# Optimization experiments

Measured on AMD Instinct MI355X. Metric: run time of the kernel, lower is better.

Reference implementation:

```python
import jax, jax.numpy as jnp
import numpy as np
import math

D_MODEL = 1024
H = 16
D_K = D_MODEL // H
SEQ = 4096
NEG = -1000000000.0  # mask constant from the original code


def setup_inputs() -> dict:
    key = jax.random.key(0)
    ks = jax.random.split(key, 7)
    return {
        "Q": jax.random.normal(ks[0], (SEQ, D_MODEL), dtype=jnp.float32),
        "K": jax.random.normal(ks[1], (SEQ, D_MODEL), dtype=jnp.float32),
        "V": jax.random.normal(ks[2], (SEQ, D_MODEL), dtype=jnp.float32),
        "W_Q": jax.random.normal(ks[3], (H, D_MODEL, D_K), dtype=jnp.float32),
        "W_K": jax.random.normal(ks[4], (H, D_MODEL, D_K), dtype=jnp.float32),
        "W_V": jax.random.normal(ks[5], (H, D_MODEL, D_K), dtype=jnp.float32),
        "W_O": jax.random.normal(ks[6], (D_MODEL, D_MODEL), dtype=jnp.float32),
        "mask": 1,
    }


def reference(Q, K, V, W_Q, W_K, W_V, W_O, mask):
    d_k = W_Q.shape[-1]
    s = Q.shape[0]
    # batched per-head projections: [h, s, d_k]
    Qh = jnp.einsum("sd,hdk->hsk", Q, W_Q)
    Kh = jnp.einsum("sd,hdk->hsk", K, W_K)
    Vh = jnp.einsum("sd,hdk->hsk", V, W_V)
    # scores: [h, s_q, s_k]
    scores = jnp.einsum("hqk,hsk->hqs", Qh, Kh) / math.sqrt(d_k)
    if mask:
        # faithful to torch: tril(scores) + triu(ones, 1) * -1e9
        lower = jnp.tril(jnp.ones((s, s), dtype=scores.dtype))
        upper = jnp.triu(jnp.ones((s, s), dtype=scores.dtype), k=1)
        scores = scores * lower + upper * NEG
    attn = jax.nn.softmax(scores, axis=-1)
    heads = jnp.einsum("hqs,hsk->hqk", attn, Vh)  # [h, s, d_k]
    # concat heads along feature dim in head order -> [s, h*d_k]
    concat = jnp.transpose(heads, (1, 0, 2)).reshape(s, -1)
    return concat @ W_O
```

## Files before the change

### kernel.cpp

```cpp
#include <hip/hip_runtime.h>
#include <hip/hip_bf16.h>

constexpr int S      = 4096;
constexpr int DMODEL = 1024;
constexpr int H      = 16;
constexpr int DK     = 64;

typedef __attribute__((ext_vector_type(8))) short          short8;
typedef __attribute__((ext_vector_type(4))) short          short4v;
typedef __attribute__((ext_vector_type(4))) float          float4v;
typedef __attribute__((ext_vector_type(4))) unsigned short ushort4v;
typedef __attribute__((ext_vector_type(8))) unsigned short ushort8;

__device__ __forceinline__ unsigned short f2bf(float x) {
    unsigned u = __builtin_bit_cast(unsigned, x);
    u += 0x7FFFu + ((u >> 16) & 1u);
    return (unsigned short)(u >> 16);
}
__device__ __forceinline__ float bf2f(unsigned short h) {
    unsigned u = ((unsigned)h) << 16;
    return __builtin_bit_cast(float, u);
}

__global__ __launch_bounds__(256) void split_inputs(const float* __restrict__ Q,
                                                    const float* __restrict__ K,
                                                    const float* __restrict__ V,
                                                    unsigned short* __restrict__ QH,
                                                    unsigned short* __restrict__ QL,
                                                    unsigned short* __restrict__ KH,
                                                    unsigned short* __restrict__ KL,
                                                    unsigned short* __restrict__ Vb)
{
    const int z = blockIdx.z;
    const size_t base = ((size_t)blockIdx.x * 256 + threadIdx.x) * 8;
    const float* src = (z == 0) ? Q : (z == 1) ? K : V;
    const float4 a = *(const float4*)(src + base);
    const float4 b = *(const float4*)(src + base + 4);
    const float xs[8] = {a.x, a.y, a.z, a.w, b.x, b.y, b.z, b.w};
    ushort8 hv, lv;
#pragma unroll
    for (int j = 0; j < 8; ++j) {
        const unsigned short h = f2bf(xs[j]);
        hv[j] = h;
        lv[j] = f2bf(xs[j] - bf2f(h));
    }
    if (z == 0)      { *(ushort8*)(QH + base) = hv; *(ushort8*)(QL + base) = lv; }
    else if (z == 1) { *(ushort8*)(KH + base) = hv; *(ushort8*)(KL + base) = lv; }
    else             { *(ushort8*)(Vb + base) = hv; }
}

__global__ __launch_bounds__(256) void conv_k(const float* __restrict__ Kc,
                                              unsigned short* __restrict__ KH,
                                              unsigned short* __restrict__ KL)
{
    const size_t base = ((size_t)blockIdx.x * 256 + threadIdx.x) * 8;
    const float4 a = *(const float4*)(Kc + base);
    const float4 b = *(const float4*)(Kc + base + 4);
    const float xs[8] = {a.x, a.y, a.z, a.w, b.x, b.y, b.z, b.w};
    ushort8 hv, lv;
#pragma unroll
    for (int j = 0; j < 8; ++j) {
        const unsigned short h = f2bf(xs[j]);
        hv[j] = h;
        lv[j] = f2bf(xs[j] - bf2f(h));
    }
    *(ushort8*)(KH + base) = hv;
    *(ushort8*)(KL + base) = lv;
}

__global__ __launch_bounds__(256) void transpose_v(const float* __restrict__ Vc,
                                                   unsigned short* __restrict__ Vt)
{
    __shared__ unsigned short Ts[64][68];
    const int t  = threadIdx.x;
    const int s0 = blockIdx.x * 64;
    const int n0 = blockIdx.y * 64;
#pragma unroll
    for (int i = 0; i < 4; ++i) {
        const int row = (t >> 4) + i * 16;
        const int col = (t & 15) * 4;
        const float4 v = *(const float4*)&Vc[(size_t)(s0 + row) * 1024 + n0 + col];
        Ts[row][col + 0] = f2bf(v.x); Ts[row][col + 1] = f2bf(v.y);
        Ts[row][col + 2] = f2bf(v.z); Ts[row][col + 3] = f2bf(v.w);
    }
    __syncthreads();
#pragma unroll
    for (int i = 0; i < 4; ++i) {
        const int n  = (t >> 4) + i * 16;
        const int sb = (t & 15) * 4;
        ushort4v v;
#pragma unroll
        for (int j = 0; j < 4; ++j) v[j] = Ts[sb + j][n];
        *(ushort4v*)&Vt[(size_t)(n0 + n) * 4096 + s0 + sb] = v;
    }
}

__global__ __launch_bounds__(256) void transpose_w(const float* __restrict__ in,
                                                   unsigned short* __restrict__ oh,
                                                   unsigned short* __restrict__ ol,
                                                   int z_mult, int rstride)
{
    __shared__ float Ts[64][65];
    const int t  = threadIdx.x;
    const int z  = blockIdx.z;
    const int r0 = blockIdx.x * 64;
    const float* src = in + (size_t)z * z_mult;
#pragma unroll
    for (int i = 0; i < 4; ++i) {
        const int row = (t >> 4) + i * 16;
        const int col = (t & 15) * 4;
        const float4 v = *(const float4*)&src[(size_t)(r0 + row) * rstride + col];
        Ts[row][col + 0] = v.x; Ts[row][col + 1] = v.y;
        Ts[row][col + 2] = v.z; Ts[row][col + 3] = v.w;
    }
    __syncthreads();
#pragma unroll
    for (int i = 0; i < 4; ++i) {
        const int c  = (t >> 4) + i * 16;
        const int rb = (t & 15) * 4;
        ushort4v hv, lv;
#pragma unroll
        for (int j = 0; j < 4; ++j) {
            const float x = Ts[rb + j][c];
            const unsigned short h = f2bf(x);
            hv[j] = h;
            lv[j] = f2bf(x - bf2f(h));
        }
        const size_t o = (size_t)(z * 64 + c) * 1024 + r0 + rb;
        *(ushort4v*)&oh[o] = hv;
        if (ol) *(ushort4v*)&ol[o] = lv;
    }
}

template <bool SPLIT>
__device__ __forceinline__ void gemm_core(unsigned short* __restrict__ sm,
                                          const unsigned short* __restrict__ Ah,
                                          const unsigned short* __restrict__ Al,
                                          const unsigned short* __restrict__ Bh,
                                          const unsigned short* __restrict__ Bl,
                                          float* __restrict__ C,
                                          int m0, int n0)
{
    unsigned short* AsH = sm;
    unsigned short* BsH = sm + 4096;
    unsigned short* AsL = sm + 8192;
    unsigned short* BsL = sm + 12288;

    const int t    = threadIdx.x;
    const int wave = t >> 6;
    const int lane = t & 63;
    const int quad = lane >> 4;
    const int l15  = lane & 15;
    const int wm   = (wave & 1) * 64;
    const int wn   = (wave >> 1) * 64;

    float4v acc[4][4];
#pragma unroll
    for (int mi = 0; mi < 4; ++mi)
#pragma unroll
        for (int ni = 0; ni < 4; ++ni)
#pragma unroll
            for (int r = 0; r < 4; ++r) acc[mi][ni][r] = 0.f;

    for (int k0 = 0; k0 < 1024; k0 += 32) {
        __syncthreads();
#pragma unroll
        for (int i = 0; i < 2; ++i) {
            const int c   = t + 256 * i;
            const int row = c >> 2;
            const int kc  = (c & 3) * 8;
            *(ushort8*)&AsH[row * 32 + kc] =
                *(const ushort8*)&Ah[(size_t)(m0 + row) * 1024 + k0 + kc];
            *(ushort8*)&BsH[row * 32 + kc] =
                *(const ushort8*)&Bh[(size_t)(n0 + row) * 1024 + k0 + kc];
            if (SPLIT) {
                *(ushort8*)&AsL[row * 32 + kc] =
                    *(const ushort8*)&Al[(size_t)(m0 + row) * 1024 + k0 + kc];
                *(ushort8*)&BsL[row * 32 + kc] =
                    *(const ushort8*)&Bl[(size_t)(n0 + row) * 1024 + k0 + kc];
            }
        }
        __syncthreads();

        short8 afh[4], bfh[4], afl[4], bfl[4];
#pragma unroll
        for (int mi = 0; mi < 4; ++mi)
            afh[mi] = *(const short8*)&AsH[(wm + mi * 16 + l15) * 32 + quad * 8];
#pragma unroll
        for (int ni = 0; ni < 4; ++ni)
            bfh[ni] = *(const short8*)&BsH[(wn + ni * 16 + l15) * 32 + quad * 8];
        if (SPLIT) {
#pragma unroll
            for (int mi = 0; mi < 4; ++mi)
                afl[mi] = *(const short8*)&AsL[(wm + mi * 16 + l15) * 32 + quad * 8];
#pragma unroll
            for (int ni = 0; ni < 4; ++ni)
                bfl[ni] = *(const short8*)&BsL[(wn + ni * 16 + l15) * 32 + quad * 8];
        }

#pragma unroll
        for (int mi = 0; mi < 4; ++mi)
#pragma unroll
            for (int ni = 0; ni < 4; ++ni) {
                acc[mi][ni] = __builtin_amdgcn_mfma_f32_16x16x32_bf16(
                    afh[mi], bfh[ni], acc[mi][ni], 0, 0, 0);
                if (SPLIT) {
                    acc[mi][ni] = __builtin_amdgcn_mfma_f32_16x16x32_bf16(
                        afh[mi], bfl[ni], acc[mi][ni], 0, 0, 0);
                    acc[mi][ni] = __builtin_amdgcn_mfma_f32_16x16x32_bf16(
                        afl[mi], bfh[ni], acc[mi][ni], 0, 0, 0);
                }
            }
    }

#pragma unroll
    for (int mi = 0; mi < 4; ++mi)
#pragma unroll
        for (int r = 0; r < 4; ++r) {
            const int m = m0 + wm + mi * 16 + quad * 4 + r;
            float* cp = C + (size_t)m * 1024 + n0 + wn + l15;
#pragma unroll
            for (int ni = 0; ni < 4; ++ni) cp[ni * 16] = acc[mi][ni][r];
        }
}

__global__ __launch_bounds__(256) void proj_mfma(
    const unsigned short* __restrict__ XqH, const unsigned short* __restrict__ XqL,
    const unsigned short* __restrict__ XkH, const unsigned short* __restrict__ XkL,
    const unsigned short* __restrict__ Xv,
    const unsigned short* __restrict__ WqtH, const unsigned short* __restrict__ WqtL,
    const unsigned short* __restrict__ WktH, const unsigned short* __restrict__ WktL,
    const unsigned short* __restrict__ Wvt,
    float* __restrict__ Qc, float* __restrict__ Kc, float* __restrict__ Vc)
{
    __shared__ __align__(16) unsigned short smem[4 * 4096];
    const int m0 = blockIdx.x * 128, n0 = blockIdx.y * 128;
    if (blockIdx.z == 0)
        gemm_core<true>(smem, XqH, XqL, WqtH, WqtL, Qc, m0, n0);
    else if (blockIdx.z == 1)
        gemm_core<true>(smem, XkH, XkL, WktH, WktL, Kc, m0, n0);
    else
        gemm_core<false>(smem, Xv, nullptr, Wvt, nullptr, Vc, m0, n0);
}

__global__ __launch_bounds__(256) void out_gemm_mfma(
    const unsigned short* __restrict__ Ocb,
    const unsigned short* __restrict__ WOt,
    float* __restrict__ out)
{
    __shared__ __align__(16) unsigned short smem[2 * 4096];
    gemm_core<false>(smem, Ocb, nullptr, WOt, nullptr, out,
                     blockIdx.x * 128, blockIdx.y * 128);
}

__global__ __launch_bounds__(256) void attn_mfma(const float* __restrict__ Qc,
                                                 const unsigned short* __restrict__ KHg,
                                                 const unsigned short* __restrict__ KLg,
                                                 const unsigned short* __restrict__ Vtg,
                                                 unsigned short* __restrict__ Ocb)
{
    __shared__ __align__(16) short Khi[64][72];
    __shared__ __align__(16) short Klo[64][72];
    __shared__ __align__(16) short Vts[64][72];
    __shared__ __align__(16) short Pb[4][16][72];

    const int bid = blockIdx.x;
    const int h   = bid & 15;
    const int qt  = 63 - (bid >> 4);
    const int q0  = qt * 64;

    const int t    = threadIdx.x;
    const int wave = t >> 6;
    const int lane = t & 63;
    const int quad = lane >> 4;
    const int l15  = lane & 15;

    short8 qhi[2], qlo[2];
    {
        const int qrow = q0 + wave * 16 + l15;
        const float* qp = Qc + (size_t)qrow * DMODEL + h * 64 + quad * 8;
#pragma unroll
        for (int ks = 0; ks < 2; ++ks) {
            float4 a = *(const float4*)(qp + ks * 32);
            float4 b = *(const float4*)(qp + ks * 32 + 4);
            const float xs[8] = {a.x, a.y, a.z, a.w, b.x, b.y, b.z, b.w};
#pragma unroll
            for (int j = 0; j < 8; ++j) {
                const unsigned short hi = f2bf(xs[j]);
                const unsigned short lo = f2bf(xs[j] - bf2f(hi));
                qhi[ks][j] = (short)hi;
                qlo[ks][j] = (short)lo;
            }
        }
    }

    short8 bones;
    {
        const short ob = (l15 == 0) ? (short)0x3F80 : (short)0;
#pragma unroll
        for (int j = 0; j < 8; ++j) bones[j] = ob;
    }

    float m_r[4] = {-1e30f, -1e30f, -1e30f, -1e30f};
    float4v lacc;
    float4v oacc[4];
#pragma unroll
    for (int r = 0; r < 4; ++r) lacc[r] = 0.f;
#pragma unroll
    for (int nt = 0; nt < 4; ++nt)
#pragma unroll
        for (int r = 0; r < 4; ++r) oacc[nt][r] = 0.f;

    const int srow = t >> 3;
    const int soff = (t & 7) * 8;

    ushort8 kh[2], kl[2], vt[2];
#pragma unroll
    for (int i = 0; i < 2; ++i) {
        const int row = srow + 32 * i;
        kh[i] = *(const ushort8*)&KHg[(size_t)row * 1024 + h * 64 + soff];
        kl[i] = *(const ushort8*)&KLg[(size_t)row * 1024 + h * 64 + soff];
        vt[i] = *(const ushort8*)&Vtg[(size_t)(h * 64 + row) * 4096 + soff];
    }

    for (int jt = 0; jt <= qt; ++jt) {
        const int j0 = jt * 64;
#pragma unroll
        for (int i = 0; i < 2; ++i) {
            const int row = srow + 32 * i;
            *(ushort8*)&Khi[row][soff] = kh[i];
            *(ushort8*)&Klo[row][soff] = kl[i];
            *(ushort8*)&Vts[row][soff] = vt[i];
        }
        __syncthreads();

        if (jt < qt) {
            const int jn = j0 + 64;
#pragma unroll
            for (int i = 0; i < 2; ++i) {
                const int row = srow + 32 * i;
                kh[i] = *(const ushort8*)&KHg[(size_t)(jn + row) * 1024 + h * 64 + soff];
                kl[i] = *(const ushort8*)&KLg[(size_t)(jn + row) * 1024 + h * 64 + soff];
                vt[i] = *(const ushort8*)&Vtg[(size_t)(h * 64 + row) * 4096 + jn + soff];
            }
        }

        float4v sacc[4];
#pragma unroll
        for (int nt = 0; nt < 4; ++nt)
#pragma unroll
            for (int r = 0; r < 4; ++r) sacc[nt][r] = 0.f;
#pragma unroll
        for (int nt = 0; nt < 4; ++nt) {
            const int key = nt * 16 + l15;
#pragma unroll
            for (int ks = 0; ks < 2; ++ks) {
                const short8 bh = *(const short8*)&Khi[key][ks * 32 + quad * 8];
                const short8 bl = *(const short8*)&Klo[key][ks * 32 + quad * 8];
                sacc[nt] = __builtin_amdgcn_mfma_f32_16x16x32_bf16(qhi[ks], bh, sacc[nt], 0, 0, 0);
                sacc[nt] = __builtin_amdgcn_mfma_f32_16x16x32_bf16(qhi[ks], bl, sacc[nt], 0, 0, 0);
                sacc[nt] = __builtin_amdgcn_mfma_f32_16x16x32_bf16(qlo[ks], bh, sacc[nt], 0, 0, 0);
            }
        }

#pragma unroll
        for (int nt = 0; nt < 4; ++nt) {
            const int jg = j0 + nt * 16 + l15;
#pragma unroll
            for (int r = 0; r < 4; ++r) {
                const int qg = q0 + wave * 16 + quad * 4 + r;
                const float v = sacc[nt][r] * 0.125f;
                sacc[nt][r] = (jg > qg) ? -1e9f : v;
            }
        }

        float rmax[4];
#pragma unroll
        for (int r = 0; r < 4; ++r)
            rmax[r] = fmaxf(fmaxf(sacc[0][r], sacc[1][r]), fmaxf(sacc[2][r], sacc[3][r]));
#pragma unroll
        for (int off = 1; off < 16; off <<= 1)
#pragma unroll
            for (int r = 0; r < 4; ++r)
                rmax[r] = fmaxf(rmax[r], __shfl_xor(rmax[r], off));

        float alpha[4];
#pragma unroll
        for (int r = 0; r < 4; ++r) {
            const float mn = fmaxf(m_r[r], rmax[r]);
            alpha[r] = __expf(m_r[r] - mn);
            m_r[r] = mn;
        }

#pragma unroll
        for (int nt = 0; nt < 4; ++nt)
#pragma unroll
            for (int r = 0; r < 4; ++r)
                sacc[nt][r] = __expf(sacc[nt][r] - m_r[r]);

#pragma unroll
        for (int r = 0; r < 4; ++r) lacc[r] *= alpha[r];
#pragma unroll
        for (int nt = 0; nt < 4; ++nt)
#pragma unroll
            for (int r = 0; r < 4; ++r)
                oacc[nt][r] *= alpha[r];

#pragma unroll
        for (int nt = 0; nt < 4; ++nt)
#pragma unroll
            for (int r = 0; r < 4; ++r)
                Pb[wave][quad * 4 + r][nt * 16 + l15] = (short)f2bf(sacc[nt][r]);
        __asm__ volatile("s_waitcnt lgkmcnt(0)" ::: "memory");

        short8 af[2];
        af[0] = *(const short8*)&Pb[wave][l15][quad * 8];
        af[1] = *(const short8*)&Pb[wave][l15][32 + quad * 8];
#pragma unroll
        for (int nt = 0; nt < 4; ++nt) {
            const int dk = nt * 16 + l15;
#pragma unroll
            for (int ks = 0; ks < 2; ++ks) {
                const short8 bv = *(const short8*)&Vts[dk][ks * 32 + quad * 8];
                oacc[nt] = __builtin_amdgcn_mfma_f32_16x16x32_bf16(af[ks], bv, oacc[nt], 0, 0, 0);
            }
        }
        lacc = __builtin_amdgcn_mfma_f32_16x16x32_bf16(af[0], bones, lacc, 0, 0, 0);
        lacc = __builtin_amdgcn_mfma_f32_16x16x32_bf16(af[1], bones, lacc, 0, 0, 0);
        __syncthreads();
    }

#pragma unroll
    for (int r = 0; r < 4; ++r) {
        const float lsum = __shfl(lacc[r], (lane & 48));
        const float inv  = 1.0f / lsum;
        const int qg = q0 + wave * 16 + quad * 4 + r;
        unsigned short* op = Ocb + (size_t)qg * DMODEL + h * 64 + l15;
#pragma unroll
        for (int nt = 0; nt < 4; ++nt)
            op[nt * 16] = f2bf(oacc[nt][r] * inv);
    }
}

extern "C" void kernel_launch(void* const* d_in, const int* in_sizes, int n_in,
                              void* d_out, int out_size, void* d_ws, size_t ws_size,
                              hipStream_t stream)
{
    const float* Q  = (const float*)d_in[0];
    const float* K  = (const float*)d_in[1];
    const float* V  = (const float*)d_in[2];
    const float* WQ = (const float*)d_in[3];
    const float* WK = (const float*)d_in[4];
    const float* WV = (const float*)d_in[5];
    const float* WO = (const float*)d_in[6];

    float* out = (float*)d_out;

    const size_t SD4 = (size_t)S * DMODEL * 4;
    const size_t SD2 = (size_t)S * DMODEL * 2;
    const size_t W2  = (size_t)DMODEL * DMODEL * 2;
    char* p = (char*)d_ws;
    auto take = [&](size_t b) { char* r = p; p += b; return r; };

    float* Qc = (float*)take(SD4);
    float* Kc = (float*)take(SD4);
    float* Vc = (float*)take(SD4);
    unsigned short* XqH = (unsigned short*)take(SD2);
    unsigned short* XqL = (unsigned short*)take(SD2);
    unsigned short* XkH = (unsigned short*)take(SD2);
    unsigned short* XkL = (unsigned short*)take(SD2);
    unsigned short* Xv  = (unsigned short*)take(SD2);
    unsigned short* WqtH = (unsigned short*)take(W2);
    unsigned short* WqtL = (unsigned short*)take(W2);
    unsigned short* WktH = (unsigned short*)take(W2);
    unsigned short* WktL = (unsigned short*)take(W2);
    unsigned short* Wvt  = (unsigned short*)take(W2);
    unsigned short* WOt  = (unsigned short*)take(W2);
    unsigned short* Ocb  = (unsigned short*)take(SD2);
    unsigned short* KHg = XqH;
    unsigned short* KLg = XqL;
    unsigned short* Vtg = Xv;

    split_inputs<<<dim3(2048, 1, 3), 256, 0, stream>>>(Q, K, V,
                                                       XqH, XqL, XkH, XkL, Xv);
    transpose_w<<<dim3(16, 1, 16), 256, 0, stream>>>(WQ, WqtH, WqtL, 65536, 64);
    transpose_w<<<dim3(16, 1, 16), 256, 0, stream>>>(WK, WktH, WktL, 65536, 64);
    transpose_w<<<dim3(16, 1, 16), 256, 0, stream>>>(WV, Wvt, nullptr, 65536, 64);
    transpose_w<<<dim3(16, 1, 16), 256, 0, stream>>>(WO, WOt, nullptr, 64, 1024);
    proj_mfma<<<dim3(S / 128, DMODEL / 128, 3), 256, 0, stream>>>(
        XqH, XqL, XkH, XkL, Xv, WqtH, WqtL, WktH, WktL, Wvt, Qc, Kc, Vc);
    conv_k<<<dim3(2048), 256, 0, stream>>>(Kc, KHg, KLg);
    transpose_v<<<dim3(S / 64, DMODEL / 64), 256, 0, stream>>>(Vc, Vtg);
    attn_mfma<<<dim3((S / 64) * H), 256, 0, stream>>>(Qc, KHg, KLg, Vtg, Ocb);
    out_gemm_mfma<<<dim3(S / 128, DMODEL / 128), 256, 0, stream>>>(Ocb, WOt, out);
}
```

Measured before the change: 355.3 us.

## Use direct global-to-LDS loads in projection GEMM and exp2 softmax

The projection GEMM now stages tiles with global_load_lds, which writes straight into shared memory and skips the register round-trip. The attention kernel folds log2(e) into the score scale so it can use the hardware exp2 instruction. It also applies the causal mask compare only on diagonal tiles, leaving a plain scale multiply elsewhere. The LDS addressing changes from row*32+kc to a per-wave linear layout, which may not match the fragment read pattern unless the two coincide.

```diff
diff --git a/kernel.cpp b/kernel.cpp
--- a/kernel.cpp
+++ b/kernel.cpp
@@ -20,6 +20,13 @@
 __device__ __forceinline__ float bf2f(unsigned short h) {
     unsigned u = ((unsigned)h) << 16;
     return __builtin_bit_cast(float, u);
+}
+__device__ __forceinline__ float fexp2(float x) { return __builtin_amdgcn_exp2f(x); }
+
+__device__ __forceinline__ void gl_lds16(const unsigned short* g, unsigned short* l) {
+    __builtin_amdgcn_global_load_lds(
+        (const __attribute__((address_space(1))) unsigned int*)g,
+        (__attribute__((address_space(3))) unsigned int*)l, 16, 0, 0);
 }
 
 __global__ __launch_bounds__(256) void split_inputs(const float* __restrict__ Q,
@@ -169,15 +176,12 @@
             const int c   = t + 256 * i;
             const int row = c >> 2;
             const int kc  = (c & 3) * 8;
-            *(ushort8*)&AsH[row * 32 + kc] =
-                *(const ushort8*)&Ah[(size_t)(m0 + row) * 1024 + k0 + kc];
-            *(ushort8*)&BsH[row * 32 + kc] =
-                *(const ushort8*)&Bh[(size_t)(n0 + row) * 1024 + k0 + kc];
+            const int lb  = (i * 256 + wave * 64) * 8;
+            gl_lds16(&Ah[(size_t)(m0 + row) * 1024 + k0 + kc], AsH + lb);
+            gl_lds16(&Bh[(size_t)(n0 + row) * 1024 + k0 + kc], BsH + lb);
             if (SPLIT) {
-                *(ushort8*)&AsL[row * 32 + kc] =
-                    *(const ushort8*)&Al[(size_t)(m0 + row) * 1024 + k0 + kc];
-                *(ushort8*)&BsL[row * 32 + kc] =
-                    *(const ushort8*)&Bl[(size_t)(n0 + row) * 1024 + k0 + kc];
+                gl_lds16(&Al[(size_t)(m0 + row) * 1024 + k0 + kc], AsL + lb);
+                gl_lds16(&Bl[(size_t)(n0 + row) * 1024 + k0 + kc], BsL + lb);
             }
         }
         __syncthreads();
@@ -301,6 +305,8 @@
         for (int j = 0; j < 8; ++j) bones[j] = ob;
     }
 
+    constexpr float SCL = 0.18033688011112042f;
+
     float m_r[4] = {-1e30f, -1e30f, -1e30f, -1e30f};
     float4v lacc;
     float4v oacc[4];
@@ -363,15 +369,23 @@
             }
         }
 
-#pragma unroll
-        for (int nt = 0; nt < 4; ++nt) {
-            const int jg = j0 + nt * 16 + l15;
-#pragma unroll
-            for (int r = 0; r < 4; ++r) {
-                const int qg = q0 + wave * 16 + quad * 4 + r;
-                const float v = sacc[nt][r] * 0.125f;
-                sacc[nt][r] = (jg > qg) ? -1e9f : v;
-            }
+        if (jt == qt) {
+#pragma unroll
+            for (int nt = 0; nt < 4; ++nt) {
+                const int jg = j0 + nt * 16 + l15;
+#pragma unroll
+                for (int r = 0; r < 4; ++r) {
+                    const int qg = q0 + wave * 16 + quad * 4 + r;
+                    const float v = sacc[nt][r] * SCL;
+                    sacc[nt][r] = (jg > qg) ? -1e9f : v;
+                }
+            }
+        } else {
+#pragma unroll
+            for (int nt = 0; nt < 4; ++nt)
+#pragma unroll
+                for (int r = 0; r < 4; ++r)
+                    sacc[nt][r] *= SCL;
         }
 
         float rmax[4];
@@ -388,7 +402,7 @@
 #pragma unroll
         for (int r = 0; r < 4; ++r) {
             const float mn = fmaxf(m_r[r], rmax[r]);
-            alpha[r] = __expf(m_r[r] - mn);
+            alpha[r] = fexp2(m_r[r] - mn);
             m_r[r] = mn;
         }
 
@@ -396,7 +410,7 @@
         for (int nt = 0; nt < 4; ++nt)
 #pragma unroll
             for (int r = 0; r < 4; ++r)
-                sacc[nt][r] = __expf(sacc[nt][r] - m_r[r]);
+                sacc[nt][r] = fexp2(sacc[nt][r] - m_r[r]);
 
 #pragma unroll
         for (int r = 0; r < 4; ++r) lacc[r] *= alpha[r];
```

Result: no change. 351.2 us (-1.2%).
